# Performance work log

Measured on AMD Instinct MI355X. Metric: run time of the kernel, lower is better.

The kernel has to match this reference:

```python
import jax, jax.numpy as jnp
import numpy as np

N_NODES = 100000
N_EDGES = 3300000
IN_DIM = 512
HID = 512
OUT_DIM = 256
BATCH = 16


def setup_inputs() -> dict:
    key = jax.random.key(0)
    ks = jax.random.split(key, 12)
    embedding = jax.random.normal(ks[0], (N_NODES, IN_DIM), dtype=jnp.float32)
    rows = jax.random.randint(ks[1], (N_EDGES,), 0, N_NODES, dtype=jnp.int32)
    cols = jax.random.randint(ks[2], (N_EDGES,), 0, N_NODES, dtype=jnp.int32)
    adj_vals = jax.random.uniform(ks[3], (N_EDGES,), dtype=jnp.float32)
    stdv = 1.0 / np.sqrt(HID)
    W1 = jax.random.uniform(ks[4], (IN_DIM, HID), minval=-stdv, maxval=stdv, dtype=jnp.float32)
    b1 = jax.random.uniform(ks[5], (HID,), minval=-stdv, maxval=stdv, dtype=jnp.float32)
    W2 = jax.random.uniform(ks[6], (HID, HID), minval=-stdv, maxval=stdv, dtype=jnp.float32)
    b2 = jax.random.uniform(ks[7], (HID,), minval=-stdv, maxval=stdv, dtype=jnp.float32)
    stdf = 1.0 / np.sqrt(HID)
    Wf = jax.random.uniform(ks[8], (HID, OUT_DIM), minval=-stdf, maxval=stdf, dtype=jnp.float32)
    bf = jax.random.uniform(ks[9], (OUT_DIM,), minval=-stdf, maxval=stdf, dtype=jnp.float32)
    lang_idx = jax.random.randint(ks[10], (BATCH,), 0, N_NODES, dtype=jnp.int32)
    return {"embedding": embedding, "rows": rows, "cols": cols, "adj_vals": adj_vals,
            "W1": W1, "b1": b1, "W2": W2, "b2": b2, "Wf": Wf, "bf": bf,
            "lang_idx": lang_idx}


def reference(embedding, rows, cols, adj_vals, W1, b1, W2, b2, Wf, bf, lang_idx):
    n = embedding.shape[0]

    def spmm(x):
        # sparse COO adj @ x : gather source rows, scale, scatter-add to dest rows
        return jax.ops.segment_sum(adj_vals[:, None] * x[cols], rows, num_segments=n)

    # GCN layer 1: relu(adj @ (X W1) + b1); dropout is identity in eval mode
    h = jax.nn.relu(spmm(embedding @ W1) + b1)
    # GCN layer 2
    h = jax.nn.relu(spmm(h @ W2) + b2)
    # final linear, then select requested language nodes
    out = h @ Wf + bf
    return out[lang_idx]
```

## Files before the change

kernel.cpp:

```cpp
#include <hip/hip_runtime.h>
#include <hip/hip_bf16.h>

#define IN_DIM 512
#define HID    512
#define OUT_DIM 256

#define CAP_S1 1024
#define BKT    128
#define NBMAX  64
#define BM_WORDS 3328

__global__ void zero_init_kernel(const int* __restrict__ lang, int nB,
                                 const float* __restrict__ b1,
                                 const float* __restrict__ b2,
                                 const float* __restrict__ bf,
                                 unsigned* __restrict__ bmL,
                                 unsigned* __restrict__ zwords, int nZ,
                                 float* __restrict__ h1acc,
                                 float* __restrict__ h2acc,
                                 float* __restrict__ outp) {
    const int T = blockDim.x * gridDim.x;
    int t = blockIdx.x * blockDim.x + threadIdx.x;

    if (blockIdx.x == 0) {
        for (int i = threadIdx.x; i < BM_WORDS; i += blockDim.x) bmL[i] = 0u;
        __syncthreads();
        if (threadIdx.x < nB) {
            int n = lang[threadIdx.x];
            atomicOr(&bmL[n >> 5], 1u << (n & 31));
        }
    }
    for (int i = t; i < nZ; i += T) zwords[i] = 0u;
    const float4* b1v = (const float4*)b1;
    float4* h1v = (float4*)h1acc;
    for (int i = t; i < CAP_S1 * (HID / 4); i += T)
        h1v[i] = b1v[i & (HID / 4 - 1)];
    const float4* b2v = (const float4*)b2;
    float4* h2v = (float4*)h2acc;
    for (int i = t; i < nB * (HID / 4); i += T)
        h2v[i] = b2v[i & (HID / 4 - 1)];
    const float4* bfv = (const float4*)bf;
    float4* ov = (float4*)outp;
    for (int i = t; i < nB * (OUT_DIM / 4); i += T)
        ov[i] = bfv[i & (OUT_DIM / 4 - 1)];
}

__global__ void scan_lang_kernel(const int* __restrict__ rows,
                                 const int* __restrict__ cols,
                                 const float* __restrict__ vals,
                                 const int* __restrict__ lang,
                                 int nE, int nB,
                                 const unsigned* __restrict__ bmL,
                                 unsigned* __restrict__ bmS,
                                 int* __restrict__ bcount,
                                 int2* __restrict__ L2b) {
    __shared__ int slang[NBMAX];
    for (int i = threadIdx.x; i < nB; i += blockDim.x) slang[i] = lang[i];
    __syncthreads();
    int t = blockIdx.x * blockDim.x + threadIdx.x;
    int e0 = t * 4;
    if (e0 >= nE) return;
    int rr[4];
    if (e0 + 3 < nE) {
        int4 r4 = ((const int4*)rows)[t];
        rr[0] = r4.x; rr[1] = r4.y; rr[2] = r4.z; rr[3] = r4.w;
    } else {
#pragma unroll
        for (int k = 0; k < 4; ++k) rr[k] = (e0 + k < nE) ? rows[e0 + k] : -1;
    }
#pragma unroll
    for (int k = 0; k < 4; ++k) {
        int e = e0 + k;
        if (e >= nE) break;
        int r = rr[k];
        if (r >= 0 && (bmL[r >> 5] & (1u << (r & 31)))) {
            int c = cols[e];
            float v = vals[e];
            atomicOr(&bmS[c >> 5], 1u << (c & 31));
            for (int b = 0; b < nB; ++b) {
                if (slang[b] == r) {
                    int p = atomicAdd(&bcount[b], 1);
                    if (p < BKT) L2b[b * BKT + p] = make_int2(c, __float_as_int(v));
                }
            }
        }
    }
}

__global__ void assign_slots_kernel(const unsigned* __restrict__ bmS, int nN,
                                    int* __restrict__ slot, int* __restrict__ cnt1) {
    int n = blockIdx.x * blockDim.x + threadIdx.x;
    if (n < nN && (bmS[n >> 5] & (1u << (n & 31)))) slot[n] = atomicAdd(cnt1, 1);
}

__global__ void scan_s1_kernel(const int* __restrict__ rows,
                               const int* __restrict__ cols,
                               const float* __restrict__ vals,
                               int nE,
                               const unsigned* __restrict__ bmS,
                               const int* __restrict__ slot,
                               int* __restrict__ scount,
                               int2* __restrict__ L1b) {
    int t = blockIdx.x * blockDim.x + threadIdx.x;
    int e0 = t * 4;
    if (e0 >= nE) return;
    int rr[4];
    if (e0 + 3 < nE) {
        int4 r4 = ((const int4*)rows)[t];
        rr[0] = r4.x; rr[1] = r4.y; rr[2] = r4.z; rr[3] = r4.w;
    } else {
#pragma unroll
        for (int k = 0; k < 4; ++k) rr[k] = (e0 + k < nE) ? rows[e0 + k] : -1;
    }
#pragma unroll
    for (int k = 0; k < 4; ++k) {
        int e = e0 + k;
        if (e >= nE) break;
        int r = rr[k];
        if (r >= 0 && (bmS[r >> 5] & (1u << (r & 31)))) {
            int s = slot[r];
            if ((unsigned)s < CAP_S1) {
                int p = atomicAdd(&scount[s], 1);
                if (p < BKT) L1b[s * BKT + p] = make_int2(cols[e], __float_as_int(vals[e]));
            }
        }
    }
}

__global__ void agg_x_kernel(const int2* __restrict__ L1b,
                             const int* __restrict__ scount,
                             const int* __restrict__ cnt1,
                             const float* __restrict__ X,
                             float* __restrict__ agg1) {
    int s = blockIdx.x;
    int cnt = *cnt1; if (cnt > CAP_S1) cnt = CAP_S1;
    if (s >= cnt) return;
    __shared__ int2 ent[BKT];
    int n = scount[s]; if (n > BKT) n = BKT;
    for (int i = threadIdx.x; i < n; i += blockDim.x) ent[i] = L1b[s * BKT + i];
    __syncthreads();
    int tid = threadIdx.x;
    float2 acc = make_float2(0.f, 0.f);
    int i = 0;
    for (; i + 4 <= n; i += 4) {
        int2 e0 = ent[i], e1 = ent[i + 1], e2 = ent[i + 2], e3 = ent[i + 3];
        float2 f0 = ((const float2*)(X + (size_t)e0.x * IN_DIM))[tid];
        float2 f1 = ((const float2*)(X + (size_t)e1.x * IN_DIM))[tid];
        float2 f2 = ((const float2*)(X + (size_t)e2.x * IN_DIM))[tid];
        float2 f3 = ((const float2*)(X + (size_t)e3.x * IN_DIM))[tid];
        float v0 = __int_as_float(e0.y), v1 = __int_as_float(e1.y);
        float v2 = __int_as_float(e2.y), v3 = __int_as_float(e3.y);
        acc.x += f0.x * v0 + f1.x * v1 + f2.x * v2 + f3.x * v3;
        acc.y += f0.y * v0 + f1.y * v1 + f2.y * v2 + f3.y * v3;
    }
    for (; i < n; ++i) {
        int2 e = ent[i];
        float2 f = ((const float2*)(X + (size_t)e.x * IN_DIM))[tid];
        float v = __int_as_float(e.y);
        acc.x += f.x * v; acc.y += f.y * v;
    }
    ((float2*)(agg1 + (size_t)s * HID))[tid] = acc;
}

__global__ void agg_h1_kernel(const int2* __restrict__ L2b,
                              const int* __restrict__ bcount,
                              const int* __restrict__ slot,
                              const float* __restrict__ h1acc,
                              float* __restrict__ agg2) {
    int b = blockIdx.x;
    __shared__ int2 ent[BKT];
    __shared__ int sidx[BKT];
    int n = bcount[b]; if (n > BKT) n = BKT;
    for (int i = threadIdx.x; i < n; i += blockDim.x) ent[i] = L2b[b * BKT + i];
    __syncthreads();
    for (int i = threadIdx.x; i < n; i += blockDim.x) sidx[i] = slot[ent[i].x];
    __syncthreads();
    int tid = threadIdx.x;
    float2 acc = make_float2(0.f, 0.f);
    for (int i = 0; i < n; ++i) {
        int s = sidx[i];
        float2 f = ((const float2*)(h1acc + (size_t)s * HID))[tid];
        float v = __int_as_float(ent[i].y);
        acc.x += fmaxf(f.x, 0.f) * v;
        acc.y += fmaxf(f.y, 0.f) * v;
    }
    ((float2*)(agg2 + (size_t)b * HID))[tid] = acc;
}

template <int KS>
__global__ void gemm_acc_kernel(const float* __restrict__ A,
                                const float* __restrict__ W,
                                float* __restrict__ Out,
                                const int* __restrict__ cntPtr, int fixedCnt,
                                int N, int reluA) {
    int cnt = cntPtr ? *cntPtr : fixedCnt;
    if (cnt > CAP_S1) cnt = CAP_S1;
    int row0 = blockIdx.z * 16;
    if (row0 >= cnt) return;
    int k0 = blockIdx.y * KS;
    int c0 = blockIdx.x * 256;

    __shared__ float sA[16 * KS];
    constexpr int NQ = 16 * KS / 4;
    for (int idx = threadIdx.x; idx < NQ; idx += 128) {
        int j = idx / (KS / 4), q = idx % (KS / 4);
        float4 a = make_float4(0.f, 0.f, 0.f, 0.f);
        if (row0 + j < cnt) {
            a = *(const float4*)(A + (size_t)(row0 + j) * 512 + k0 + 4 * q);
            if (reluA) {
                a.x = fmaxf(a.x, 0.f); a.y = fmaxf(a.y, 0.f);
                a.z = fmaxf(a.z, 0.f); a.w = fmaxf(a.w, 0.f);
            }
        }
        *(float4*)(sA + j * KS + 4 * q) = a;
    }
    __syncthreads();

    int c = c0 + threadIdx.x;
    float acc0[16], acc1[16];
#pragma unroll
    for (int j = 0; j < 16; ++j) { acc0[j] = 0.f; acc1[j] = 0.f; }

    for (int kc = 0; kc < KS; kc += 16) {
        float wv0[16], wv1[16];
#pragma unroll
        for (int k = 0; k < 16; ++k) {
            const float* wr = W + (size_t)(k0 + kc + k) * N;
            wv0[k] = wr[c];
            wv1[k] = wr[c + 128];
        }
#pragma unroll
        for (int k = 0; k < 16; k += 4) {
#pragma unroll
            for (int j = 0; j < 16; ++j) {
                float4 a = *(const float4*)(sA + j * KS + kc + k);
                acc0[j] += a.x * wv0[k] + a.y * wv0[k + 1] + a.z * wv0[k + 2] + a.w * wv0[k + 3];
                acc1[j] += a.x * wv1[k] + a.y * wv1[k + 1] + a.z * wv1[k + 2] + a.w * wv1[k + 3];
            }
        }
    }
#pragma unroll
    for (int j = 0; j < 16; ++j) {
        if (row0 + j < cnt) {
            atomicAdd(&Out[(size_t)(row0 + j) * N + c], acc0[j]);
            atomicAdd(&Out[(size_t)(row0 + j) * N + c + 128], acc1[j]);
        }
    }
}

extern "C" void kernel_launch(void* const* d_in, const int* in_sizes, int n_in,
                              void* d_out, int out_size, void* d_ws, size_t ws_size,
                              hipStream_t stream) {
    const float* X    = (const float*)d_in[0];
    const int*   rows = (const int*)d_in[1];
    const int*   cols = (const int*)d_in[2];
    const float* vals = (const float*)d_in[3];
    const float* W1   = (const float*)d_in[4];
    const float* b1   = (const float*)d_in[5];
    const float* W2   = (const float*)d_in[6];
    const float* b2   = (const float*)d_in[7];
    const float* Wf   = (const float*)d_in[8];
    const float* bf   = (const float*)d_in[9];
    const int*   lang = (const int*)d_in[10];

    int nN = in_sizes[0] / IN_DIM;
    int nE = in_sizes[1];
    int nB = in_sizes[10];
    float* out = (float*)d_out;

    char* w = (char*)d_ws;
    unsigned* bmL  = (unsigned*)w;  w += BM_WORDS * 4;
    unsigned* zw   = (unsigned*)w;
    unsigned* bmS  = (unsigned*)w;  w += BM_WORDS * 4;
    int* cnts      = (int*)w;       w += 64 * 4;
    int* scount    = (int*)w;       w += CAP_S1 * 4;
    int* bcount    = (int*)w;       w += NBMAX * 4;
    int nZ         = (int)(((unsigned*)w) - zw);
    int* slot      = (int*)w;       w += ((size_t)nN * 4 + 255) & ~(size_t)255;
    int2* L2b      = (int2*)w;      w += (size_t)NBMAX * BKT * 8;
    int2* L1b      = (int2*)w;      w += (size_t)CAP_S1 * BKT * 8;
    float* agg1    = (float*)w;     w += (size_t)CAP_S1 * HID * 4;
    float* h1acc   = (float*)w;     w += (size_t)CAP_S1 * HID * 4;
    float* agg2    = (float*)w;     w += (size_t)NBMAX * HID * 4;
    float* h2acc   = (float*)w;     w += (size_t)NBMAX * HID * 4;

    int nT = (nE + 3) / 4;
    int eBlocks = (nT + 255) / 256;
    int nBlocks = (nN + 255) / 256;

    zero_init_kernel<<<512, 256, 0, stream>>>(lang, nB, b1, b2, bf,
                                              bmL, zw, nZ, h1acc, h2acc, out);
    scan_lang_kernel<<<eBlocks, 256, 0, stream>>>(rows, cols, vals, lang, nE, nB,
                                                  bmL, bmS, bcount, L2b);
    assign_slots_kernel<<<nBlocks, 256, 0, stream>>>(bmS, nN, slot, &cnts[0]);
    scan_s1_kernel<<<eBlocks, 256, 0, stream>>>(rows, cols, vals, nE, bmS, slot,
                                                scount, L1b);
    agg_x_kernel<<<CAP_S1, 256, 0, stream>>>(L1b, scount, &cnts[0], X, agg1);
    gemm_acc_kernel<128><<<dim3(HID / 256, 4, CAP_S1 / 16), 128, 0, stream>>>(
        agg1, W1, h1acc, &cnts[0], 0, HID, 0);
    agg_h1_kernel<<<nB, 256, 0, stream>>>(L2b, bcount, slot, h1acc, agg2);
    gemm_acc_kernel<64><<<dim3(HID / 256, 8, 1), 128, 0, stream>>>(
        agg2, W2, h2acc, nullptr, nB, HID, 0);
    gemm_acc_kernel<64><<<dim3(OUT_DIM / 256, 8, 1), 128, 0, stream>>>(
        h2acc, Wf, out, nullptr, nB, OUT_DIM, 1);
}
```

Before: 170.5 us.

## Fuse layer-2 aggregation, W2 GEMM and final linear into one tail kernel

Replaces the agg_h1 kernel and two small atomic-accumulating GEMM launches with a single per-batch-node kernel of 512 threads. It aggregates relu(h1) neighbors, multiplies by W2 with bias and relu, then applies Wf and bf, all in shared memory. This removes two launches, the intermediate agg2/h2acc buffers, their bias pre-initialization and the atomics. The cost is less parallelism: only nB blocks each read all of W2 and Wf serially.

New measurement: 140.0 us. 17.9% less time.

```diff
diff --git a/kernel.cpp b/kernel.cpp
--- a/kernel.cpp
+++ b/kernel.cpp
@@ -12,13 +12,9 @@
 
 __global__ void zero_init_kernel(const int* __restrict__ lang, int nB,
                                  const float* __restrict__ b1,
-                                 const float* __restrict__ b2,
-                                 const float* __restrict__ bf,
                                  unsigned* __restrict__ bmL,
                                  unsigned* __restrict__ zwords, int nZ,
-                                 float* __restrict__ h1acc,
-                                 float* __restrict__ h2acc,
-                                 float* __restrict__ outp) {
+                                 float* __restrict__ h1acc) {
     const int T = blockDim.x * gridDim.x;
     int t = blockIdx.x * blockDim.x + threadIdx.x;
 
@@ -35,14 +31,6 @@
     float4* h1v = (float4*)h1acc;
     for (int i = t; i < CAP_S1 * (HID / 4); i += T)
         h1v[i] = b1v[i & (HID / 4 - 1)];
-    const float4* b2v = (const float4*)b2;
-    float4* h2v = (float4*)h2acc;
-    for (int i = t; i < nB * (HID / 4); i += T)
-        h2v[i] = b2v[i & (HID / 4 - 1)];
-    const float4* bfv = (const float4*)bf;
-    float4* ov = (float4*)outp;
-    for (int i = t; i < nB * (OUT_DIM / 4); i += T)
-        ov[i] = bfv[i & (OUT_DIM / 4 - 1)];
 }
 
 __global__ void scan_lang_kernel(const int* __restrict__ rows,
@@ -162,31 +150,6 @@
     ((float2*)(agg1 + (size_t)s * HID))[tid] = acc;
 }
 
-__global__ void agg_h1_kernel(const int2* __restrict__ L2b,
-                              const int* __restrict__ bcount,
-                              const int* __restrict__ slot,
-                              const float* __restrict__ h1acc,
-                              float* __restrict__ agg2) {
-    int b = blockIdx.x;
-    __shared__ int2 ent[BKT];
-    __shared__ int sidx[BKT];
-    int n = bcount[b]; if (n > BKT) n = BKT;
-    for (int i = threadIdx.x; i < n; i += blockDim.x) ent[i] = L2b[b * BKT + i];
-    __syncthreads();
-    for (int i = threadIdx.x; i < n; i += blockDim.x) sidx[i] = slot[ent[i].x];
-    __syncthreads();
-    int tid = threadIdx.x;
-    float2 acc = make_float2(0.f, 0.f);
-    for (int i = 0; i < n; ++i) {
-        int s = sidx[i];
-        float2 f = ((const float2*)(h1acc + (size_t)s * HID))[tid];
-        float v = __int_as_float(ent[i].y);
-        acc.x += fmaxf(f.x, 0.f) * v;
-        acc.y += fmaxf(f.y, 0.f) * v;
-    }
-    ((float2*)(agg2 + (size_t)b * HID))[tid] = acc;
-}
-
 template <int KS>
 __global__ void gemm_acc_kernel(const float* __restrict__ A,
                                 const float* __restrict__ W,
@@ -246,6 +209,84 @@
             atomicAdd(&Out[(size_t)(row0 + j) * N + c + 128], acc1[j]);
         }
     }
+}
+
+__global__ void tail_kernel(const int2* __restrict__ L2b,
+                            const int* __restrict__ bcount,
+                            const int* __restrict__ slot,
+                            const float* __restrict__ h1acc,
+                            const float* __restrict__ W2,
+                            const float* __restrict__ b2,
+                            const float* __restrict__ Wf,
+                            const float* __restrict__ bf,
+                            float* __restrict__ outp) {
+    int b = blockIdx.x;
+    int tid = threadIdx.x;
+    __shared__ int2 ent[BKT];
+    __shared__ int sidx[BKT];
+    __shared__ float sagg[HID];
+    __shared__ float sh2[HID];
+    __shared__ float ppart[2][OUT_DIM];
+
+    int n = bcount[b]; if (n > BKT) n = BKT;
+    for (int i = tid; i < n; i += blockDim.x) ent[i] = L2b[b * BKT + i];
+    __syncthreads();
+    for (int i = tid; i < n; i += blockDim.x) sidx[i] = slot[ent[i].x];
+    __syncthreads();
+
+    float acc = 0.f;
+    int i = 0;
+    for (; i + 4 <= n; i += 4) {
+        int s0 = sidx[i], s1 = sidx[i + 1], s2 = sidx[i + 2], s3 = sidx[i + 3];
+        float f0 = h1acc[(size_t)s0 * HID + tid];
+        float f1 = h1acc[(size_t)s1 * HID + tid];
+        float f2 = h1acc[(size_t)s2 * HID + tid];
+        float f3 = h1acc[(size_t)s3 * HID + tid];
+        acc += fmaxf(f0, 0.f) * __int_as_float(ent[i].y)
+             + fmaxf(f1, 0.f) * __int_as_float(ent[i + 1].y)
+             + fmaxf(f2, 0.f) * __int_as_float(ent[i + 2].y)
+             + fmaxf(f3, 0.f) * __int_as_float(ent[i + 3].y);
+    }
+    for (; i < n; ++i)
+        acc += fmaxf(h1acc[(size_t)sidx[i] * HID + tid], 0.f) * __int_as_float(ent[i].y);
+    sagg[tid] = acc;
+    __syncthreads();
+
+    float a2 = b2[tid];
+    for (int k = 0; k < HID; k += 8) {
+        float w0 = W2[(size_t)(k + 0) * HID + tid];
+        float w1 = W2[(size_t)(k + 1) * HID + tid];
+        float w2 = W2[(size_t)(k + 2) * HID + tid];
+        float w3 = W2[(size_t)(k + 3) * HID + tid];
+        float w4 = W2[(size_t)(k + 4) * HID + tid];
+        float w5 = W2[(size_t)(k + 5) * HID + tid];
+        float w6 = W2[(size_t)(k + 6) * HID + tid];
+        float w7 = W2[(size_t)(k + 7) * HID + tid];
+        a2 += sagg[k + 0] * w0 + sagg[k + 1] * w1 + sagg[k + 2] * w2 + sagg[k + 3] * w3
+            + sagg[k + 4] * w4 + sagg[k + 5] * w5 + sagg[k + 6] * w6 + sagg[k + 7] * w7;
+    }
+    sh2[tid] = fmaxf(a2, 0.f);
+    __syncthreads();
+
+    int g = tid >> 8, c = tid & 255;
+    int k0 = g * 256;
+    float p = 0.f;
+    for (int k = 0; k < 256; k += 8) {
+        float w0 = Wf[(size_t)(k0 + k + 0) * OUT_DIM + c];
+        float w1 = Wf[(size_t)(k0 + k + 1) * OUT_DIM + c];
+        float w2 = Wf[(size_t)(k0 + k + 2) * OUT_DIM + c];
+        float w3 = Wf[(size_t)(k0 + k + 3) * OUT_DIM + c];
+        float w4 = Wf[(size_t)(k0 + k + 4) * OUT_DIM + c];
+        float w5 = Wf[(size_t)(k0 + k + 5) * OUT_DIM + c];
+        float w6 = Wf[(size_t)(k0 + k + 6) * OUT_DIM + c];
+        float w7 = Wf[(size_t)(k0 + k + 7) * OUT_DIM + c];
+        p += sh2[k0 + k + 0] * w0 + sh2[k0 + k + 1] * w1 + sh2[k0 + k + 2] * w2 + sh2[k0 + k + 3] * w3
+           + sh2[k0 + k + 4] * w4 + sh2[k0 + k + 5] * w5 + sh2[k0 + k + 6] * w6 + sh2[k0 + k + 7] * w7;
+    }
+    ppart[g][c] = p;
+    __syncthreads();
+    if (tid < OUT_DIM)
+        outp[(size_t)b * OUT_DIM + tid] = bf[tid] + ppart[0][tid] + ppart[1][tid];
 }
 
 extern "C" void kernel_launch(void* const* d_in, const int* in_sizes, int n_in,
@@ -281,15 +322,12 @@
     int2* L1b      = (int2*)w;      w += (size_t)CAP_S1 * BKT * 8;
     float* agg1    = (float*)w;     w += (size_t)CAP_S1 * HID * 4;
     float* h1acc   = (float*)w;     w += (size_t)CAP_S1 * HID * 4;
-    float* agg2    = (float*)w;     w += (size_t)NBMAX * HID * 4;
-    float* h2acc   = (float*)w;     w += (size_t)NBMAX * HID * 4;
 
     int nT = (nE + 3) / 4;
     int eBlocks = (nT + 255) / 256;
     int nBlocks = (nN + 255) / 256;
 
-    zero_init_kernel<<<512, 256, 0, stream>>>(lang, nB, b1, b2, bf,
-                                              bmL, zw, nZ, h1acc, h2acc, out);
+    zero_init_kernel<<<512, 256, 0, stream>>>(lang, nB, b1, bmL, zw, nZ, h1acc);
     scan_lang_kernel<<<eBlocks, 256, 0, stream>>>(rows, cols, vals, lang, nE, nB,
                                                   bmL, bmS, bcount, L2b);
     assign_slots_kernel<<<nBlocks, 256, 0, stream>>>(bmS, nN, slot, &cnts[0]);
@@ -298,9 +336,6 @@
     agg_x_kernel<<<CAP_S1, 256, 0, stream>>>(L1b, scount, &cnts[0], X, agg1);
     gemm_acc_kernel<128><<<dim3(HID / 256, 4, CAP_S1 / 16), 128, 0, stream>>>(
         agg1, W1, h1acc, &cnts[0], 0, HID, 0);
-    agg_h1_kernel<<<nB, 256, 0, stream>>>(L2b, bcount, slot, h1acc, agg2);
-    gemm_acc_kernel<64><<<dim3(HID / 256, 8, 1), 128, 0, stream>>>(
-        agg2, W2, h2acc, nullptr, nB, HID, 0);
-    gemm_acc_kernel<64><<<dim3(OUT_DIM / 256, 8, 1), 128, 0, stream>>>(
-        h2acc, Wf, out, nullptr, nB, OUT_DIM, 1);
-}
+    tail_kernel<<<nB, 512, 0, stream>>>(L2b, bcount, slot, h1acc,
+                                        W2, b2, Wf, bf, out);
+}
```

## Replace atomic split-K accumulation with per-split planes and fuse tail stages

Applied to the files above, without the earlier changes.

The layer-1 GEMM now writes each K-split partial to its own plane instead of atomically adding into a bias-initialised buffer, so the large bias fill in the init kernel goes away. The layer-2 aggregation, W2 GEMM and final linear are fused into one 1024-thread block per batch node that sums the planes, adds the bias and applies ReLU on the fly. This removes three kernel launches, the atomics and the intermediate buffers. In exchange each block reads four planes per neighbour, and the small GEMMs run in a single block per batch row with less parallelism.

New measurement: 138.8 us. 1.23x faster.

```diff
diff --git a/kernel.cpp b/kernel.cpp
--- a/kernel.cpp
+++ b/kernel.cpp
@@ -9,19 +9,14 @@
 #define BKT    128
 #define NBMAX  64
 #define BM_WORDS 3328
+#define NKS    4
+#define PLANE  ((size_t)CAP_S1 * HID)
 
 __global__ void zero_init_kernel(const int* __restrict__ lang, int nB,
-                                 const float* __restrict__ b1,
-                                 const float* __restrict__ b2,
-                                 const float* __restrict__ bf,
                                  unsigned* __restrict__ bmL,
-                                 unsigned* __restrict__ zwords, int nZ,
-                                 float* __restrict__ h1acc,
-                                 float* __restrict__ h2acc,
-                                 float* __restrict__ outp) {
+                                 unsigned* __restrict__ zwords, int nZ) {
     const int T = blockDim.x * gridDim.x;
     int t = blockIdx.x * blockDim.x + threadIdx.x;
-
     if (blockIdx.x == 0) {
         for (int i = threadIdx.x; i < BM_WORDS; i += blockDim.x) bmL[i] = 0u;
         __syncthreads();
@@ -31,18 +26,6 @@
         }
     }
     for (int i = t; i < nZ; i += T) zwords[i] = 0u;
-    const float4* b1v = (const float4*)b1;
-    float4* h1v = (float4*)h1acc;
-    for (int i = t; i < CAP_S1 * (HID / 4); i += T)
-        h1v[i] = b1v[i & (HID / 4 - 1)];
-    const float4* b2v = (const float4*)b2;
-    float4* h2v = (float4*)h2acc;
-    for (int i = t; i < nB * (HID / 4); i += T)
-        h2v[i] = b2v[i & (HID / 4 - 1)];
-    const float4* bfv = (const float4*)bf;
-    float4* ov = (float4*)outp;
-    for (int i = t; i < nB * (OUT_DIM / 4); i += T)
-        ov[i] = bfv[i & (OUT_DIM / 4 - 1)];
 }
 
 __global__ void scan_lang_kernel(const int* __restrict__ rows,
@@ -162,56 +145,23 @@
     ((float2*)(agg1 + (size_t)s * HID))[tid] = acc;
 }
 
-__global__ void agg_h1_kernel(const int2* __restrict__ L2b,
-                              const int* __restrict__ bcount,
-                              const int* __restrict__ slot,
-                              const float* __restrict__ h1acc,
-                              float* __restrict__ agg2) {
-    int b = blockIdx.x;
-    __shared__ int2 ent[BKT];
-    __shared__ int sidx[BKT];
-    int n = bcount[b]; if (n > BKT) n = BKT;
-    for (int i = threadIdx.x; i < n; i += blockDim.x) ent[i] = L2b[b * BKT + i];
-    __syncthreads();
-    for (int i = threadIdx.x; i < n; i += blockDim.x) sidx[i] = slot[ent[i].x];
-    __syncthreads();
-    int tid = threadIdx.x;
-    float2 acc = make_float2(0.f, 0.f);
-    for (int i = 0; i < n; ++i) {
-        int s = sidx[i];
-        float2 f = ((const float2*)(h1acc + (size_t)s * HID))[tid];
-        float v = __int_as_float(ent[i].y);
-        acc.x += fmaxf(f.x, 0.f) * v;
-        acc.y += fmaxf(f.y, 0.f) * v;
-    }
-    ((float2*)(agg2 + (size_t)b * HID))[tid] = acc;
-}
-
-template <int KS>
-__global__ void gemm_acc_kernel(const float* __restrict__ A,
-                                const float* __restrict__ W,
-                                float* __restrict__ Out,
-                                const int* __restrict__ cntPtr, int fixedCnt,
-                                int N, int reluA) {
-    int cnt = cntPtr ? *cntPtr : fixedCnt;
-    if (cnt > CAP_S1) cnt = CAP_S1;
+__global__ void gemm_plane_kernel(const float* __restrict__ A,
+                                  const float* __restrict__ W,
+                                  float* __restrict__ h1p,
+                                  const int* __restrict__ cntPtr) {
+    int cnt = *cntPtr; if (cnt > CAP_S1) cnt = CAP_S1;
     int row0 = blockIdx.z * 16;
     if (row0 >= cnt) return;
+    const int KS = 128, N = HID;
     int k0 = blockIdx.y * KS;
     int c0 = blockIdx.x * 256;
 
     __shared__ float sA[16 * KS];
-    constexpr int NQ = 16 * KS / 4;
-    for (int idx = threadIdx.x; idx < NQ; idx += 128) {
+    for (int idx = threadIdx.x; idx < 16 * KS / 4; idx += 128) {
         int j = idx / (KS / 4), q = idx % (KS / 4);
         float4 a = make_float4(0.f, 0.f, 0.f, 0.f);
-        if (row0 + j < cnt) {
+        if (row0 + j < cnt)
             a = *(const float4*)(A + (size_t)(row0 + j) * 512 + k0 + 4 * q);
-            if (reluA) {
-                a.x = fmaxf(a.x, 0.f); a.y = fmaxf(a.y, 0.f);
-                a.z = fmaxf(a.z, 0.f); a.w = fmaxf(a.w, 0.f);
-            }
-        }
         *(float4*)(sA + j * KS + 4 * q) = a;
     }
     __syncthreads();
@@ -239,13 +189,94 @@
             }
         }
     }
+    float* plane = h1p + (size_t)blockIdx.y * PLANE;
 #pragma unroll
     for (int j = 0; j < 16; ++j) {
         if (row0 + j < cnt) {
-            atomicAdd(&Out[(size_t)(row0 + j) * N + c], acc0[j]);
-            atomicAdd(&Out[(size_t)(row0 + j) * N + c + 128], acc1[j]);
-        }
-    }
+            plane[(size_t)(row0 + j) * N + c] = acc0[j];
+            plane[(size_t)(row0 + j) * N + c + 128] = acc1[j];
+        }
+    }
+}
+
+__global__ void tail_kernel(const int2* __restrict__ L2b,
+                            const int* __restrict__ bcount,
+                            const int* __restrict__ slot,
+                            const float* __restrict__ h1p,
+                            const float* __restrict__ b1,
+                            const float* __restrict__ W2,
+                            const float* __restrict__ b2,
+                            const float* __restrict__ Wf,
+                            const float* __restrict__ bf,
+                            float* __restrict__ outp) {
+    int b = blockIdx.x;
+    int tid = threadIdx.x;
+    __shared__ int2 ent[BKT];
+    __shared__ int sidx[BKT];
+    __shared__ float saggp[2][HID];
+    __shared__ float sagg[HID];
+    __shared__ float ph2p[2][HID];
+    __shared__ float sh2[HID];
+    __shared__ float ppart[4][OUT_DIM];
+
+    int n = bcount[b]; if (n > BKT) n = BKT;
+    if (tid < BKT && tid < n) ent[tid] = L2b[b * BKT + tid];
+    __syncthreads();
+    if (tid < BKT && tid < n) sidx[tid] = slot[ent[tid].x];
+    __syncthreads();
+
+    {
+        int c = tid & (HID - 1), g = tid >> 9;
+        float b1c = b1[c];
+        float acc = 0.f;
+        int i = g;
+        for (; i + 2 < n; i += 4) {
+            int sA_ = sidx[i], sB_ = sidx[i + 2];
+            const float* pa = h1p + (size_t)sA_ * HID + c;
+            const float* pb = h1p + (size_t)sB_ * HID + c;
+            float ha = pa[0] + pa[PLANE] + pa[2 * PLANE] + pa[3 * PLANE] + b1c;
+            float hb = pb[0] + pb[PLANE] + pb[2 * PLANE] + pb[3 * PLANE] + b1c;
+            acc += fmaxf(ha, 0.f) * __int_as_float(ent[i].y)
+                 + fmaxf(hb, 0.f) * __int_as_float(ent[i + 2].y);
+        }
+        for (; i < n; i += 2) {
+            int s = sidx[i];
+            const float* pa = h1p + (size_t)s * HID + c;
+            float ha = pa[0] + pa[PLANE] + pa[2 * PLANE] + pa[3 * PLANE] + b1c;
+            acc += fmaxf(ha, 0.f) * __int_as_float(ent[i].y);
+        }
+        saggp[g][c] = acc;
+    }
+    __syncthreads();
+    if (tid < HID) sagg[tid] = saggp[0][tid] + saggp[1][tid];
+    __syncthreads();
+
+    {
+        int c = tid & (HID - 1), kh = tid >> 9;
+        int k0 = kh * 256;
+        float a = (kh == 0) ? b2[c] : 0.f;
+#pragma unroll 8
+        for (int k = 0; k < 256; ++k)
+            a += sagg[k0 + k] * W2[(size_t)(k0 + k) * HID + c];
+        ph2p[kh][c] = a;
+    }
+    __syncthreads();
+    if (tid < HID) sh2[tid] = fmaxf(ph2p[0][tid] + ph2p[1][tid], 0.f);
+    __syncthreads();
+
+    {
+        int c = tid & (OUT_DIM - 1), kq = tid >> 8;
+        int k0 = kq * 128;
+        float p = 0.f;
+#pragma unroll 8
+        for (int k = 0; k < 128; ++k)
+            p += sh2[k0 + k] * Wf[(size_t)(k0 + k) * OUT_DIM + c];
+        ppart[kq][c] = p;
+    }
+    __syncthreads();
+    if (tid < OUT_DIM)
+        outp[(size_t)b * OUT_DIM + tid] =
+            bf[tid] + ppart[0][tid] + ppart[1][tid] + ppart[2][tid] + ppart[3][tid];
 }
 
 extern "C" void kernel_launch(void* const* d_in, const int* in_sizes, int n_in,
@@ -280,27 +311,21 @@
     int2* L2b      = (int2*)w;      w += (size_t)NBMAX * BKT * 8;
     int2* L1b      = (int2*)w;      w += (size_t)CAP_S1 * BKT * 8;
     float* agg1    = (float*)w;     w += (size_t)CAP_S1 * HID * 4;
-    float* h1acc   = (float*)w;     w += (size_t)CAP_S1 * HID * 4;
-    float* agg2    = (float*)w;     w += (size_t)NBMAX * HID * 4;
-    float* h2acc   = (float*)w;     w += (size_t)NBMAX * HID * 4;
+    float* h1p     = (float*)w;     w += (size_t)NKS * PLANE * 4;
 
     int nT = (nE + 3) / 4;
     int eBlocks = (nT + 255) / 256;
     int nBlocks = (nN + 255) / 256;
 
-    zero_init_kernel<<<512, 256, 0, stream>>>(lang, nB, b1, b2, bf,
-                                              bmL, zw, nZ, h1acc, h2acc, out);
+    zero_init_kernel<<<64, 256, 0, stream>>>(lang, nB, bmL, zw, nZ);
     scan_lang_kernel<<<eBlocks, 256, 0, stream>>>(rows, cols, vals, lang, nE, nB,
                                                   bmL, bmS, bcount, L2b);
     assign_slots_kernel<<<nBlocks, 256, 0, stream>>>(bmS, nN, slot, &cnts[0]);
     scan_s1_kernel<<<eBlocks, 256, 0, stream>>>(rows, cols, vals, nE, bmS, slot,
                                                 scount, L1b);
     agg_x_kernel<<<CAP_S1, 256, 0, stream>>>(L1b, scount, &cnts[0], X, agg1);
-    gemm_acc_kernel<128><<<dim3(HID / 256, 4, CAP_S1 / 16), 128, 0, stream>>>(
-        agg1, W1, h1acc, &cnts[0], 0, HID, 0);
-    agg_h1_kernel<<<nB, 256, 0, stream>>>(L2b, bcount, slot, h1acc, agg2);
-    gemm_acc_kernel<64><<<dim3(HID / 256, 8, 1), 128, 0, stream>>>(
-        agg2, W2, h2acc, nullptr, nB, HID, 0);
-    gemm_acc_kernel<64><<<dim3(OUT_DIM / 256, 8, 1), 128, 0, stream>>>(
-        h2acc, Wf, out, nullptr, nB, OUT_DIM, 1);
-}
+    gemm_plane_kernel<<<dim3(HID / 256, NKS, CAP_S1 / 16), 128, 0, stream>>>(
+        agg1, W1, h1p, &cnts[0]);
+    tail_kernel<<<nB, 1024, 0, stream>>>(L2b, bcount, slot, h1p,
+                                         b1, W2, b2, Wf, bf, out);
+}
```
